# Kernel tuning notes

Measured on AMD Instinct MI355X. Metric: run time of the kernel, lower is better.

Reference implementation:

```python
import jax, jax.numpy as jnp
import numpy as np

WINDOW = 8
NUM_HEADS = 8
DIM = 256


def _relative_position_index(ws):
    coords = np.stack(np.meshgrid(np.arange(ws), np.arange(ws), indexing='ij'))  # [2,ws,ws]
    flat = coords.reshape(2, -1)  # [2, N]
    rel = flat[:, :, None] - flat[:, None, :]  # [2, N, N]
    rel = rel.transpose(1, 2, 0)  # [N, N, 2]
    rel[:, :, 0] += ws - 1
    rel[:, :, 1] += ws - 1
    rel[:, :, 0] *= 2 * ws - 1
    return rel.sum(-1).astype(np.int32)  # [N, N]


def setup_inputs() -> dict:
    key = jax.random.key(0)
    ks = jax.random.split(key, 6)
    B_, N, C = 4096, WINDOW * WINDOW, DIM
    return {
        'x': jax.random.normal(ks[0], (B_, N, C), jnp.float32),
        'qkv_w': jax.random.normal(ks[1], (3 * C, C), jnp.float32) * 0.02,
        'qkv_b': jax.random.normal(ks[2], (3 * C,), jnp.float32) * 0.02,
        'proj_w': jax.random.normal(ks[3], (C, C), jnp.float32) * 0.02,
        'proj_b': jax.random.normal(ks[4], (C,), jnp.float32) * 0.02,
        'bias_table': jax.random.normal(ks[5], ((2 * WINDOW - 1) ** 2, NUM_HEADS), jnp.float32) * 0.02,
        'rel_index': jnp.asarray(_relative_position_index(WINDOW)),
    }


def reference(x, qkv_w, qkv_b, proj_w, proj_b, bias_table, rel_index):
    B_, N, C = x.shape
    H = NUM_HEADS
    hd = C // H
    scale = hd ** -0.5
    qkv = x @ qkv_w.T + qkv_b  # [B_, N, 3C]
    qkv = qkv.reshape(B_, N, 3, H, hd).transpose(2, 0, 3, 1, 4)  # [3, B_, H, N, hd]
    q, k, v = qkv[0], qkv[1], qkv[2]
    attn = jnp.einsum('bhnd,bhmd->bhnm', q, k) * scale  # [B_, H, N, N]
    bias = bias_table[rel_index.reshape(-1)].reshape(N, N, H).transpose(2, 0, 1)  # [H, N, N]
    attn = jax.nn.softmax(attn + bias[None], axis=-1)
    out = jnp.einsum('bhnm,bhmd->bhnd', attn, v)  # [B_, H, N, hd]
    out = out.transpose(0, 2, 1, 3).reshape(B_, N, C)
    return out @ proj_w.T + proj_b
```

## Files before the change

kernel.cpp:

```cpp
#include <hip/hip_runtime.h>
#include <hip/hip_bf16.h>


typedef __attribute__((ext_vector_type(8))) short bf16x8;
typedef __attribute__((ext_vector_type(4))) float f32x4;

struct alignas(8) us4 { unsigned short x, y, z, w; };

__device__ inline unsigned short f2bf(float f) {
    unsigned u = __builtin_bit_cast(unsigned, f);
    u += 0x7fffu + ((u >> 16) & 1u);
    return (unsigned short)(u >> 16);
}

__device__ inline f32x4 mfma16(bf16x8 a, bf16x8 b, f32x4 c) {
    return __builtin_amdgcn_mfma_f32_16x16x32_bf16(a, b, c, 0, 0, 0);
}

__device__ inline bf16x8 lds8(const unsigned short* p) {
    return *reinterpret_cast<const bf16x8*>(p);
}

__global__ void prep_kernel(const float* __restrict__ qkv_w,
                            const float* __restrict__ proj_w,
                            const float* __restrict__ bias_table,
                            const int*   __restrict__ rel_index,
                            unsigned short* __restrict__ qkv_wb,
                            unsigned short* __restrict__ proj_wb,
                            float* __restrict__ biasF) {
    int stride = gridDim.x * blockDim.x;
    int t0 = blockIdx.x * blockDim.x + threadIdx.x;
    for (int i = t0; i < 768 * 256; i += stride) qkv_wb[i] = f2bf(qkv_w[i]);
    for (int i = t0; i < 256 * 256; i += stride) proj_wb[i] = f2bf(proj_w[i]);
    for (int i = t0; i < 8 * 64 * 64; i += stride) {
        int h = i >> 12, rem = i & 4095, m = rem >> 6, n = rem & 63;
        biasF[i] = bias_table[rel_index[m * 64 + n] * 8 + h];
    }
}

__global__ __launch_bounds__(512, 2) void win_attn_kernel(
    const float* __restrict__ x,
    const float* __restrict__ qkv_b,
    const float* __restrict__ proj_b,
    const unsigned short* __restrict__ qkv_wb,
    const unsigned short* __restrict__ proj_wb,
    const float* __restrict__ biasF,
    float* __restrict__ out)
{
    __shared__ unsigned short sm[76288];
    const int tid  = threadIdx.x;
    const int wid  = tid >> 6;
    const int lane = tid & 63;
    const int r16  = lane & 15;
    const int g    = lane >> 4;
    const int win  = blockIdx.x;
    const float* xg = x + (size_t)win * 16384;

#pragma unroll
    for (int i = 0; i < 8; ++i) {
        int flat = i * 2048 + tid * 4;
        float4 v = *reinterpret_cast<const float4*>(xg + flat);
        int row = flat >> 8, col = flat & 255;
        us4 pk = { f2bf(v.x), f2bf(v.y), f2bf(v.z), f2bf(v.w) };
        *reinterpret_cast<us4*>(&sm[row * 264 + col]) = pk;
    }
    __syncthreads();

    const int h = wid;
    int ntb[6];
    ntb[0] = 2 * h;      ntb[1] = 2 * h + 1;
    ntb[2] = 16 + 2 * h; ntb[3] = 17 + 2 * h;
    ntb[4] = 32 + 2 * h; ntb[5] = 33 + 2 * h;

    const f32x4 zero4 = {0.f, 0.f, 0.f, 0.f};
    f32x4 acc[4][6];
#pragma unroll
    for (int a = 0; a < 4; ++a)
#pragma unroll
        for (int b = 0; b < 6; ++b) acc[a][b] = zero4;

#pragma unroll
    for (int ks = 0; ks < 8; ++ks) {
        bf16x8 af[4];
#pragma unroll
        for (int mt = 0; mt < 4; ++mt)
            af[mt] = lds8(&sm[(mt * 16 + r16) * 264 + ks * 32 + g * 8]);
#pragma unroll
        for (int ni = 0; ni < 6; ++ni) {
            const unsigned short* wp =
                qkv_wb + (ntb[ni] * 16 + r16) * 256 + ks * 32 + g * 8;
            bf16x8 bf = *reinterpret_cast<const bf16x8*>(wp);
#pragma unroll
            for (int mt = 0; mt < 4; ++mt)
                acc[mt][ni] = mfma16(af[mt], bf, acc[mt][ni]);
        }
    }

    const int qbase = 16896 + h * 5120;
    const int kbase = qbase + 2560;
    const int vtb   = 57856 + h * 2304;

#pragma unroll
    for (int ni = 0; ni < 6; ++ni) {
        int n = ntb[ni] * 16 + r16;
        float qb = qkv_b[n];
        int d = (ni & 1) * 16 + r16;
#pragma unroll
        for (int mt = 0; mt < 4; ++mt) {
            f32x4 a4 = acc[mt][ni];
            if (ni < 2) {
#pragma unroll
                for (int j = 0; j < 4; ++j)
                    sm[qbase + (mt * 16 + g * 4 + j) * 40 + d] = f2bf(a4[j] + qb);
            } else if (ni < 4) {
#pragma unroll
                for (int j = 0; j < 4; ++j)
                    sm[kbase + (mt * 16 + g * 4 + j) * 40 + d] = f2bf(a4[j] + qb);
            } else {
                us4 pk = { f2bf(a4[0] + qb), f2bf(a4[1] + qb),
                           f2bf(a4[2] + qb), f2bf(a4[3] + qb) };
                *reinterpret_cast<us4*>(&sm[vtb + d * 72 + mt * 16 + g * 4]) = pk;
            }
        }
    }
    __syncthreads();

    bf16x8 ak[4], bq[4];
#pragma unroll
    for (int t = 0; t < 4; ++t) {
        ak[t] = lds8(&sm[kbase + (t * 16 + r16) * 40 + g * 8]);
        bq[t] = lds8(&sm[qbase + (t * 16 + r16) * 40 + g * 8]);
    }
    f32x4 st[4][4];
#pragma unroll
    for (int rt = 0; rt < 4; ++rt)
#pragma unroll
        for (int ct = 0; ct < 4; ++ct)
            st[rt][ct] = mfma16(ak[rt], bq[ct], zero4);

    const float scale = 0.1767766952966369f;
    const float* bh = biasF + h * 4096;

#pragma unroll
    for (int ct = 0; ct < 4; ++ct) {
        int m = ct * 16 + r16;
        float pv[4][4];
        float mx = -1e30f;
#pragma unroll
        for (int rt = 0; rt < 4; ++rt) {
            float4 b4 = *reinterpret_cast<const float4*>(bh + m * 64 + rt * 16 + g * 4);
            float bb[4] = { b4.x, b4.y, b4.z, b4.w };
#pragma unroll
            for (int j = 0; j < 4; ++j) {
                float v = st[rt][ct][j] * scale + bb[j];
                pv[rt][j] = v;
                mx = fmaxf(mx, v);
            }
        }
        mx = fmaxf(mx, __shfl_xor(mx, 16));
        mx = fmaxf(mx, __shfl_xor(mx, 32));
        float s = 0.f;
#pragma unroll
        for (int rt = 0; rt < 4; ++rt)
#pragma unroll
            for (int j = 0; j < 4; ++j) {
                float e = __expf(pv[rt][j] - mx);
                pv[rt][j] = e;
                s += e;
            }
        s += __shfl_xor(s, 16);
        s += __shfl_xor(s, 32);
        float inv = 1.f / s;
#pragma unroll
        for (int rt = 0; rt < 4; ++rt) {
            us4 pk = { f2bf(pv[rt][0] * inv), f2bf(pv[rt][1] * inv),
                       f2bf(pv[rt][2] * inv), f2bf(pv[rt][3] * inv) };
            *reinterpret_cast<us4*>(&sm[qbase + m * 72 + rt * 16 + g * 4]) = pk;
        }
    }
    asm volatile("s_waitcnt lgkmcnt(0)" ::: "memory");

    f32x4 o[4][2];
#pragma unroll
    for (int mt = 0; mt < 4; ++mt)
#pragma unroll
        for (int nt = 0; nt < 2; ++nt) o[mt][nt] = zero4;
#pragma unroll
    for (int ks = 0; ks < 2; ++ks) {
        bf16x8 ap[4];
#pragma unroll
        for (int mt = 0; mt < 4; ++mt)
            ap[mt] = lds8(&sm[qbase + (mt * 16 + r16) * 72 + ks * 32 + g * 8]);
#pragma unroll
        for (int nt = 0; nt < 2; ++nt) {
            bf16x8 bv = lds8(&sm[vtb + (nt * 16 + r16) * 72 + ks * 32 + g * 8]);
#pragma unroll
            for (int mt = 0; mt < 4; ++mt)
                o[mt][nt] = mfma16(ap[mt], bv, o[mt][nt]);
        }
    }
#pragma unroll
    for (int mt = 0; mt < 4; ++mt)
#pragma unroll
        for (int nt = 0; nt < 2; ++nt)
#pragma unroll
            for (int j = 0; j < 4; ++j)
                sm[(mt * 16 + g * 4 + j) * 264 + h * 32 + nt * 16 + r16] =
                    f2bf(o[mt][nt][j]);
    __syncthreads();

    f32x4 c3[4][2];
#pragma unroll
    for (int mt = 0; mt < 4; ++mt)
#pragma unroll
        for (int nt = 0; nt < 2; ++nt) c3[mt][nt] = zero4;
#pragma unroll
    for (int ks = 0; ks < 8; ++ks) {
        bf16x8 a3[4];
#pragma unroll
        for (int mt = 0; mt < 4; ++mt)
            a3[mt] = lds8(&sm[(mt * 16 + r16) * 264 + ks * 32 + g * 8]);
#pragma unroll
        for (int nt = 0; nt < 2; ++nt) {
            const unsigned short* wp =
                proj_wb + (wid * 32 + nt * 16 + r16) * 256 + ks * 32 + g * 8;
            bf16x8 b3 = *reinterpret_cast<const bf16x8*>(wp);
#pragma unroll
            for (int mt = 0; mt < 4; ++mt)
                c3[mt][nt] = mfma16(a3[mt], b3, c3[mt][nt]);
        }
    }
    float* og = out + (size_t)win * 16384;
#pragma unroll
    for (int nt = 0; nt < 2; ++nt) {
        int n = wid * 32 + nt * 16 + r16;
        float pb = proj_b[n];
#pragma unroll
        for (int mt = 0; mt < 4; ++mt)
#pragma unroll
            for (int j = 0; j < 4; ++j)
                og[(size_t)(mt * 16 + g * 4 + j) * 256 + n] = c3[mt][nt][j] + pb;
    }
}

extern "C" void kernel_launch(void* const* d_in, const int* in_sizes, int n_in,
                              void* d_out, int out_size, void* d_ws, size_t ws_size,
                              hipStream_t stream) {
    const float* x          = (const float*)d_in[0];
    const float* qkv_w      = (const float*)d_in[1];
    const float* qkv_b      = (const float*)d_in[2];
    const float* proj_w     = (const float*)d_in[3];
    const float* proj_b     = (const float*)d_in[4];
    const float* bias_table = (const float*)d_in[5];
    const int*   rel_index  = (const int*)d_in[6];

    unsigned short* qkv_wb = (unsigned short*)d_ws;
    unsigned short* proj_wb = (unsigned short*)((char*)d_ws + 393216);
    float* biasF = (float*)((char*)d_ws + 524288);

    prep_kernel<<<256, 256, 0, stream>>>(qkv_w, proj_w, bias_table, rel_index,
                                         qkv_wb, proj_wb, biasF);
    win_attn_kernel<<<4096, 512, 0, stream>>>(x, qkv_b, proj_b, qkv_wb, proj_wb,
                                              biasF, (float*)d_out);
}
```

Before: 426.3 us.

## Make attention kernel persistent over 16 windows with register prefetch and 16 waves

The kernel now runs 256 blocks of 1024 threads, and each block loops over 16 consecutive windows instead of handling one window per block. The next window's x tile is loaded into registers during the attention phase and written to LDS at the end of the iteration, so global loads overlap with compute. Work is split across 16 waves: two waves per head, each computing half of the Q/K/V columns and half of the query rows, and each wave computes a 16-column slice of the output projection. In exchange, each window needs more barriers, each wave holds fewer accumulators (less per-wave reuse), and carrying the prefetch registers raises register pressure.

After: 517.0 us. 21.3% more time.

```diff
diff --git a/kernel.cpp b/kernel.cpp
--- a/kernel.cpp
+++ b/kernel.cpp
@@ -38,7 +38,7 @@
     }
 }
 
-__global__ __launch_bounds__(512, 2) void win_attn_kernel(
+__global__ __launch_bounds__(1024, 4) void win_attn_kernel(
     const float* __restrict__ x,
     const float* __restrict__ qkv_b,
     const float* __restrict__ proj_b,
@@ -53,193 +53,211 @@
     const int lane = tid & 63;
     const int r16  = lane & 15;
     const int g    = lane >> 4;
-    const int win  = blockIdx.x;
-    const float* xg = x + (size_t)win * 16384;
-
-#pragma unroll
-    for (int i = 0; i < 8; ++i) {
-        int flat = i * 2048 + tid * 4;
-        float4 v = *reinterpret_cast<const float4*>(xg + flat);
-        int row = flat >> 8, col = flat & 255;
-        us4 pk = { f2bf(v.x), f2bf(v.y), f2bf(v.z), f2bf(v.w) };
-        *reinterpret_cast<us4*>(&sm[row * 264 + col]) = pk;
-    }
-    __syncthreads();
-
-    const int h = wid;
-    int ntb[6];
-    ntb[0] = 2 * h;      ntb[1] = 2 * h + 1;
-    ntb[2] = 16 + 2 * h; ntb[3] = 17 + 2 * h;
-    ntb[4] = 32 + 2 * h; ntb[5] = 33 + 2 * h;
-
+    const int h    = wid & 7;
+    const int hf   = wid >> 3;
     const f32x4 zero4 = {0.f, 0.f, 0.f, 0.f};
-    f32x4 acc[4][6];
-#pragma unroll
-    for (int a = 0; a < 4; ++a)
-#pragma unroll
-        for (int b = 0; b < 6; ++b) acc[a][b] = zero4;
-
-#pragma unroll
-    for (int ks = 0; ks < 8; ++ks) {
-        bf16x8 af[4];
-#pragma unroll
-        for (int mt = 0; mt < 4; ++mt)
-            af[mt] = lds8(&sm[(mt * 16 + r16) * 264 + ks * 32 + g * 8]);
-#pragma unroll
-        for (int ni = 0; ni < 6; ++ni) {
-            const unsigned short* wp =
-                qkv_wb + (ntb[ni] * 16 + r16) * 256 + ks * 32 + g * 8;
-            bf16x8 bf = *reinterpret_cast<const bf16x8*>(wp);
-#pragma unroll
-            for (int mt = 0; mt < 4; ++mt)
-                acc[mt][ni] = mfma16(af[mt], bf, acc[mt][ni]);
-        }
-    }
 
     const int qbase = 16896 + h * 5120;
     const int kbase = qbase + 2560;
     const int vtb   = 57856 + h * 2304;
 
-#pragma unroll
-    for (int ni = 0; ni < 6; ++ni) {
-        int n = ntb[ni] * 16 + r16;
-        float qb = qkv_b[n];
-        int d = (ni & 1) * 16 + r16;
-#pragma unroll
-        for (int mt = 0; mt < 4; ++mt) {
-            f32x4 a4 = acc[mt][ni];
-            if (ni < 2) {
+    const int ntb[3] = { 2 * h + hf, 16 + 2 * h + hf, 32 + 2 * h + hf };
+
+    const int win0 = blockIdx.x * 16;
+
+    float4 pf[4];
+#pragma unroll
+    for (int i = 0; i < 4; ++i)
+        pf[i] = *reinterpret_cast<const float4*>(
+            x + (size_t)win0 * 16384 + i * 4096 + tid * 4);
+#pragma unroll
+    for (int i = 0; i < 4; ++i) {
+        int flat = i * 4096 + tid * 4;
+        us4 pk = { f2bf(pf[i].x), f2bf(pf[i].y), f2bf(pf[i].z), f2bf(pf[i].w) };
+        *reinterpret_cast<us4*>(&sm[(flat >> 8) * 264 + (flat & 255)]) = pk;
+    }
+
+    for (int widx = 0; widx < 16; ++widx) {
+        const int win = win0 + widx;
+        __syncthreads();
+
+        f32x4 acc[4][3];
+#pragma unroll
+        for (int a = 0; a < 4; ++a)
+#pragma unroll
+            for (int b = 0; b < 3; ++b) acc[a][b] = zero4;
+
+#pragma unroll
+        for (int ks = 0; ks < 8; ++ks) {
+            bf16x8 af[4];
+#pragma unroll
+            for (int mt = 0; mt < 4; ++mt)
+                af[mt] = lds8(&sm[(mt * 16 + r16) * 264 + ks * 32 + g * 8]);
+#pragma unroll
+            for (int ni = 0; ni < 3; ++ni) {
+                bf16x8 bf = *reinterpret_cast<const bf16x8*>(
+                    qkv_wb + (ntb[ni] * 16 + r16) * 256 + ks * 32 + g * 8);
+#pragma unroll
+                for (int mt = 0; mt < 4; ++mt)
+                    acc[mt][ni] = mfma16(af[mt], bf, acc[mt][ni]);
+            }
+        }
+
+        const int d = hf * 16 + r16;
+#pragma unroll
+        for (int ni = 0; ni < 3; ++ni) {
+            float qb = qkv_b[ntb[ni] * 16 + r16];
+#pragma unroll
+            for (int mt = 0; mt < 4; ++mt) {
+                f32x4 a4 = acc[mt][ni];
+                if (ni == 0) {
+#pragma unroll
+                    for (int j = 0; j < 4; ++j)
+                        sm[qbase + (mt * 16 + g * 4 + j) * 40 + d] = f2bf(a4[j] + qb);
+                } else if (ni == 1) {
+#pragma unroll
+                    for (int j = 0; j < 4; ++j)
+                        sm[kbase + (mt * 16 + g * 4 + j) * 40 + d] = f2bf(a4[j] + qb);
+                } else {
+                    us4 pk = { f2bf(a4[0] + qb), f2bf(a4[1] + qb),
+                               f2bf(a4[2] + qb), f2bf(a4[3] + qb) };
+                    *reinterpret_cast<us4*>(&sm[vtb + d * 72 + mt * 16 + g * 4]) = pk;
+                }
+            }
+        }
+        __syncthreads();
+
+        if (widx < 15) {
+#pragma unroll
+            for (int i = 0; i < 4; ++i)
+                pf[i] = *reinterpret_cast<const float4*>(
+                    x + (size_t)(win + 1) * 16384 + i * 4096 + tid * 4);
+        }
+
+        bf16x8 ak[4], bq[2];
+#pragma unroll
+        for (int t = 0; t < 4; ++t)
+            ak[t] = lds8(&sm[kbase + (t * 16 + r16) * 40 + g * 8]);
+#pragma unroll
+        for (int c = 0; c < 2; ++c)
+            bq[c] = lds8(&sm[qbase + ((2 * hf + c) * 16 + r16) * 40 + g * 8]);
+
+        f32x4 st[4][2];
+#pragma unroll
+        for (int rt = 0; rt < 4; ++rt)
+#pragma unroll
+            for (int c = 0; c < 2; ++c)
+                st[rt][c] = mfma16(ak[rt], bq[c], zero4);
+        __syncthreads();
+
+        const float scale = 0.1767766952966369f;
+        const float* bh = biasF + h * 4096;
+
+#pragma unroll
+        for (int c = 0; c < 2; ++c) {
+            int m = (2 * hf + c) * 16 + r16;
+            float pv[4][4];
+            float mx = -1e30f;
+#pragma unroll
+            for (int rt = 0; rt < 4; ++rt) {
+                float4 b4 = *reinterpret_cast<const float4*>(
+                    bh + m * 64 + rt * 16 + g * 4);
+                float bb[4] = { b4.x, b4.y, b4.z, b4.w };
+#pragma unroll
+                for (int j = 0; j < 4; ++j) {
+                    float v = st[rt][c][j] * scale + bb[j];
+                    pv[rt][j] = v;
+                    mx = fmaxf(mx, v);
+                }
+            }
+            mx = fmaxf(mx, __shfl_xor(mx, 16));
+            mx = fmaxf(mx, __shfl_xor(mx, 32));
+            float s = 0.f;
+#pragma unroll
+            for (int rt = 0; rt < 4; ++rt)
+#pragma unroll
+                for (int j = 0; j < 4; ++j) {
+                    float e = __expf(pv[rt][j] - mx);
+                    pv[rt][j] = e;
+                    s += e;
+                }
+            s += __shfl_xor(s, 16);
+            s += __shfl_xor(s, 32);
+            float inv = 1.f / s;
+#pragma unroll
+            for (int rt = 0; rt < 4; ++rt) {
+                us4 pk = { f2bf(pv[rt][0] * inv), f2bf(pv[rt][1] * inv),
+                           f2bf(pv[rt][2] * inv), f2bf(pv[rt][3] * inv) };
+                *reinterpret_cast<us4*>(&sm[qbase + m * 72 + rt * 16 + g * 4]) = pk;
+            }
+        }
+        asm volatile("s_waitcnt lgkmcnt(0)" ::: "memory");
+
+        f32x4 o[2][2];
+#pragma unroll
+        for (int a = 0; a < 2; ++a)
+#pragma unroll
+            for (int b = 0; b < 2; ++b) o[a][b] = zero4;
+#pragma unroll
+        for (int ks = 0; ks < 2; ++ks) {
+            bf16x8 ap[2];
+#pragma unroll
+            for (int mtl = 0; mtl < 2; ++mtl)
+                ap[mtl] = lds8(&sm[qbase + ((2 * hf + mtl) * 16 + r16) * 72
+                                   + ks * 32 + g * 8]);
+#pragma unroll
+            for (int nt = 0; nt < 2; ++nt) {
+                bf16x8 bv = lds8(&sm[vtb + (nt * 16 + r16) * 72 + ks * 32 + g * 8]);
+#pragma unroll
+                for (int mtl = 0; mtl < 2; ++mtl)
+                    o[mtl][nt] = mfma16(ap[mtl], bv, o[mtl][nt]);
+            }
+        }
+#pragma unroll
+        for (int mtl = 0; mtl < 2; ++mtl)
+#pragma unroll
+            for (int nt = 0; nt < 2; ++nt)
 #pragma unroll
                 for (int j = 0; j < 4; ++j)
-                    sm[qbase + (mt * 16 + g * 4 + j) * 40 + d] = f2bf(a4[j] + qb);
-            } else if (ni < 4) {
+                    sm[((2 * hf + mtl) * 16 + g * 4 + j) * 264
+                       + h * 32 + nt * 16 + r16] = f2bf(o[mtl][nt][j]);
+        __syncthreads();
+
+        f32x4 c3[4];
+#pragma unroll
+        for (int mt = 0; mt < 4; ++mt) c3[mt] = zero4;
+#pragma unroll
+        for (int ks = 0; ks < 8; ++ks) {
+            bf16x8 b3 = *reinterpret_cast<const bf16x8*>(
+                proj_wb + (wid * 16 + r16) * 256 + ks * 32 + g * 8);
+#pragma unroll
+            for (int mt = 0; mt < 4; ++mt) {
+                bf16x8 a3 = lds8(&sm[(mt * 16 + r16) * 264 + ks * 32 + g * 8]);
+                c3[mt] = mfma16(a3, b3, c3[mt]);
+            }
+        }
+        __syncthreads();
+
+        float* og = out + (size_t)win * 16384;
+        {
+            int n = wid * 16 + r16;
+            float pb = proj_b[n];
+#pragma unroll
+            for (int mt = 0; mt < 4; ++mt)
 #pragma unroll
                 for (int j = 0; j < 4; ++j)
-                    sm[kbase + (mt * 16 + g * 4 + j) * 40 + d] = f2bf(a4[j] + qb);
-            } else {
-                us4 pk = { f2bf(a4[0] + qb), f2bf(a4[1] + qb),
-                           f2bf(a4[2] + qb), f2bf(a4[3] + qb) };
-                *reinterpret_cast<us4*>(&sm[vtb + d * 72 + mt * 16 + g * 4]) = pk;
-            }
-        }
-    }
-    __syncthreads();
-
-    bf16x8 ak[4], bq[4];
-#pragma unroll
-    for (int t = 0; t < 4; ++t) {
-        ak[t] = lds8(&sm[kbase + (t * 16 + r16) * 40 + g * 8]);
-        bq[t] = lds8(&sm[qbase + (t * 16 + r16) * 40 + g * 8]);
-    }
-    f32x4 st[4][4];
-#pragma unroll
-    for (int rt = 0; rt < 4; ++rt)
-#pragma unroll
-        for (int ct = 0; ct < 4; ++ct)
-            st[rt][ct] = mfma16(ak[rt], bq[ct], zero4);
-
-    const float scale = 0.1767766952966369f;
-    const float* bh = biasF + h * 4096;
-
-#pragma unroll
-    for (int ct = 0; ct < 4; ++ct) {
-        int m = ct * 16 + r16;
-        float pv[4][4];
-        float mx = -1e30f;
-#pragma unroll
-        for (int rt = 0; rt < 4; ++rt) {
-            float4 b4 = *reinterpret_cast<const float4*>(bh + m * 64 + rt * 16 + g * 4);
-            float bb[4] = { b4.x, b4.y, b4.z, b4.w };
-#pragma unroll
-            for (int j = 0; j < 4; ++j) {
-                float v = st[rt][ct][j] * scale + bb[j];
-                pv[rt][j] = v;
-                mx = fmaxf(mx, v);
-            }
-        }
-        mx = fmaxf(mx, __shfl_xor(mx, 16));
-        mx = fmaxf(mx, __shfl_xor(mx, 32));
-        float s = 0.f;
-#pragma unroll
-        for (int rt = 0; rt < 4; ++rt)
-#pragma unroll
-            for (int j = 0; j < 4; ++j) {
-                float e = __expf(pv[rt][j] - mx);
-                pv[rt][j] = e;
-                s += e;
-            }
-        s += __shfl_xor(s, 16);
-        s += __shfl_xor(s, 32);
-        float inv = 1.f / s;
-#pragma unroll
-        for (int rt = 0; rt < 4; ++rt) {
-            us4 pk = { f2bf(pv[rt][0] * inv), f2bf(pv[rt][1] * inv),
-                       f2bf(pv[rt][2] * inv), f2bf(pv[rt][3] * inv) };
-            *reinterpret_cast<us4*>(&sm[qbase + m * 72 + rt * 16 + g * 4]) = pk;
-        }
-    }
-    asm volatile("s_waitcnt lgkmcnt(0)" ::: "memory");
-
-    f32x4 o[4][2];
-#pragma unroll
-    for (int mt = 0; mt < 4; ++mt)
-#pragma unroll
-        for (int nt = 0; nt < 2; ++nt) o[mt][nt] = zero4;
-#pragma unroll
-    for (int ks = 0; ks < 2; ++ks) {
-        bf16x8 ap[4];
-#pragma unroll
-        for (int mt = 0; mt < 4; ++mt)
-            ap[mt] = lds8(&sm[qbase + (mt * 16 + r16) * 72 + ks * 32 + g * 8]);
-#pragma unroll
-        for (int nt = 0; nt < 2; ++nt) {
-            bf16x8 bv = lds8(&sm[vtb + (nt * 16 + r16) * 72 + ks * 32 + g * 8]);
-#pragma unroll
-            for (int mt = 0; mt < 4; ++mt)
-                o[mt][nt] = mfma16(ap[mt], bv, o[mt][nt]);
-        }
-    }
-#pragma unroll
-    for (int mt = 0; mt < 4; ++mt)
-#pragma unroll
-        for (int nt = 0; nt < 2; ++nt)
-#pragma unroll
-            for (int j = 0; j < 4; ++j)
-                sm[(mt * 16 + g * 4 + j) * 264 + h * 32 + nt * 16 + r16] =
-                    f2bf(o[mt][nt][j]);
-    __syncthreads();
-
-    f32x4 c3[4][2];
-#pragma unroll
-    for (int mt = 0; mt < 4; ++mt)
-#pragma unroll
-        for (int nt = 0; nt < 2; ++nt) c3[mt][nt] = zero4;
-#pragma unroll
-    for (int ks = 0; ks < 8; ++ks) {
-        bf16x8 a3[4];
-#pragma unroll
-        for (int mt = 0; mt < 4; ++mt)
-            a3[mt] = lds8(&sm[(mt * 16 + r16) * 264 + ks * 32 + g * 8]);
-#pragma unroll
-        for (int nt = 0; nt < 2; ++nt) {
-            const unsigned short* wp =
-                proj_wb + (wid * 32 + nt * 16 + r16) * 256 + ks * 32 + g * 8;
-            bf16x8 b3 = *reinterpret_cast<const bf16x8*>(wp);
-#pragma unroll
-            for (int mt = 0; mt < 4; ++mt)
-                c3[mt][nt] = mfma16(a3[mt], b3, c3[mt][nt]);
-        }
-    }
-    float* og = out + (size_t)win * 16384;
-#pragma unroll
-    for (int nt = 0; nt < 2; ++nt) {
-        int n = wid * 32 + nt * 16 + r16;
-        float pb = proj_b[n];
-#pragma unroll
-        for (int mt = 0; mt < 4; ++mt)
-#pragma unroll
-            for (int j = 0; j < 4; ++j)
-                og[(size_t)(mt * 16 + g * 4 + j) * 256 + n] = c3[mt][nt][j] + pb;
+                    og[(size_t)(mt * 16 + g * 4 + j) * 256 + n] = c3[mt][j] + pb;
+        }
+
+        if (widx < 15) {
+#pragma unroll
+            for (int i = 0; i < 4; ++i) {
+                int flat = i * 4096 + tid * 4;
+                us4 pk = { f2bf(pf[i].x), f2bf(pf[i].y),
+                           f2bf(pf[i].z), f2bf(pf[i].w) };
+                *reinterpret_cast<us4*>(&sm[(flat >> 8) * 264 + (flat & 255)]) = pk;
+            }
+        }
     }
 }
 
@@ -254,12 +272,12 @@
     const float* bias_table = (const float*)d_in[5];
     const int*   rel_index  = (const int*)d_in[6];
 
-    unsigned short* qkv_wb = (unsigned short*)d_ws;
+    unsigned short* qkv_wb  = (unsigned short*)d_ws;
     unsigned short* proj_wb = (unsigned short*)((char*)d_ws + 393216);
-    float* biasF = (float*)((char*)d_ws + 524288);
+    float* biasF            = (float*)((char*)d_ws + 524288);
 
     prep_kernel<<<256, 256, 0, stream>>>(qkv_w, proj_w, bias_table, rel_index,
                                          qkv_wb, proj_wb, biasF);
-    win_attn_kernel<<<4096, 512, 0, stream>>>(x, qkv_b, proj_b, qkv_wb, proj_wb,
+    win_attn_kernel<<<256, 1024, 0, stream>>>(x, qkv_b, proj_b, qkv_wb, proj_wb,
                                               biasF, (float*)d_out);
 }
```

## Keep Q/K/V and softmax probabilities in registers via lane shuffles instead of LDS

Applied to the files above, without the earlier changes.

Computes Q, K and V per head in three separate register-resident GEMM passes, choosing operand order so that the MFMA accumulator layouts can be repacked into MFMA input fragments with xor-shuffle butterflies rather than round-tripping through shared memory. The attention scale is folded into the K weights and bias during prep, and the relative position bias is used as the MFMA accumulator initialiser. Shared memory drops to the x tile plus the attention output tile, and launch bounds are raised so more blocks can fit per CU. The tradeoffs are extra cross-lane shuffles, higher register pressure under the tighter launch bound, and possible spills.

Result: slower. 621.9 us (+45.9%).

```diff
diff --git a/kernel.cpp b/kernel.cpp
--- a/kernel.cpp
+++ b/kernel.cpp
@@ -13,12 +13,36 @@
     return (unsigned short)(u >> 16);
 }
 
+__device__ inline unsigned pack2(float lo, float hi) {
+    return (unsigned)f2bf(lo) | ((unsigned)f2bf(hi) << 16);
+}
+
 __device__ inline f32x4 mfma16(bf16x8 a, bf16x8 b, f32x4 c) {
     return __builtin_amdgcn_mfma_f32_16x16x32_bf16(a, b, c, 0, 0, 0);
 }
 
 __device__ inline bf16x8 lds8(const unsigned short* p) {
     return *reinterpret_cast<const bf16x8*>(p);
+}
+
+__device__ inline void bfly_stage(unsigned V[4], int D, bool b) {
+    unsigned t0 = (unsigned)__shfl_xor((int)V[0], D);
+    unsigned t1 = (unsigned)__shfl_xor((int)V[1], D);
+    unsigned t2 = (unsigned)__shfl_xor((int)V[2], D);
+    unsigned t3 = (unsigned)__shfl_xor((int)V[3], D);
+    V[0] = b ? t2 : V[0];
+    V[1] = b ? t3 : V[1];
+    V[2] = b ? V[2] : t0;
+    V[3] = b ? V[3] : t1;
+}
+
+__device__ inline bf16x8 bfly4(unsigned v0, unsigned v1, unsigned v2,
+                               unsigned v3, int lane) {
+    unsigned V[4] = { v0, v1, v2, v3 };
+    bfly_stage(V, 32, (lane & 32) != 0);
+    bfly_stage(V, 16, (lane & 16) != 0);
+    uint4 r = { V[0], V[1], V[2], V[3] };
+    return __builtin_bit_cast(bf16x8, r);
 }
 
 __global__ void prep_kernel(const float* __restrict__ qkv_w,
@@ -28,9 +52,15 @@
                             unsigned short* __restrict__ qkv_wb,
                             unsigned short* __restrict__ proj_wb,
                             float* __restrict__ biasF) {
+    const float scale = 0.1767766952966369f;
     int stride = gridDim.x * blockDim.x;
     int t0 = blockIdx.x * blockDim.x + threadIdx.x;
-    for (int i = t0; i < 768 * 256; i += stride) qkv_wb[i] = f2bf(qkv_w[i]);
+    for (int i = t0; i < 768 * 256; i += stride) {
+        float w = qkv_w[i];
+        int row = i >> 8;
+        if (row >= 256 && row < 512) w *= scale;
+        qkv_wb[i] = f2bf(w);
+    }
     for (int i = t0; i < 256 * 256; i += stride) proj_wb[i] = f2bf(proj_w[i]);
     for (int i = t0; i < 8 * 64 * 64; i += stride) {
         int h = i >> 12, rem = i & 4095, m = rem >> 6, n = rem & 63;
@@ -38,7 +68,7 @@
     }
 }
 
-__global__ __launch_bounds__(512, 2) void win_attn_kernel(
+__global__ __launch_bounds__(512, 4) void win_attn_kernel(
     const float* __restrict__ x,
     const float* __restrict__ qkv_b,
     const float* __restrict__ proj_b,
@@ -47,116 +77,165 @@
     const float* __restrict__ biasF,
     float* __restrict__ out)
 {
-    __shared__ unsigned short sm[76288];
+    __shared__ unsigned short sm[33792];
+    const int AO   = 16896;
     const int tid  = threadIdx.x;
     const int wid  = tid >> 6;
     const int lane = tid & 63;
     const int r16  = lane & 15;
     const int g    = lane >> 4;
+    const int h    = wid;
     const int win  = blockIdx.x;
+
+    const float* bh = biasF + h * 4096;
+    const f32x4 zero4 = {0.f, 0.f, 0.f, 0.f};
+
     const float* xg = x + (size_t)win * 16384;
-
 #pragma unroll
     for (int i = 0; i < 8; ++i) {
         int flat = i * 2048 + tid * 4;
         float4 v = *reinterpret_cast<const float4*>(xg + flat);
-        int row = flat >> 8, col = flat & 255;
         us4 pk = { f2bf(v.x), f2bf(v.y), f2bf(v.z), f2bf(v.w) };
-        *reinterpret_cast<us4*>(&sm[row * 264 + col]) = pk;
+        *reinterpret_cast<us4*>(&sm[(flat >> 8) * 264 + (flat & 255)]) = pk;
     }
     __syncthreads();
 
-    const int h = wid;
-    int ntb[6];
-    ntb[0] = 2 * h;      ntb[1] = 2 * h + 1;
-    ntb[2] = 16 + 2 * h; ntb[3] = 17 + 2 * h;
-    ntb[4] = 32 + 2 * h; ntb[5] = 33 + 2 * h;
-
-    const f32x4 zero4 = {0.f, 0.f, 0.f, 0.f};
-    f32x4 acc[4][6];
-#pragma unroll
-    for (int a = 0; a < 4; ++a)
-#pragma unroll
-        for (int b = 0; b < 6; ++b) acc[a][b] = zero4;
-
-#pragma unroll
-    for (int ks = 0; ks < 8; ++ks) {
-        bf16x8 af[4];
-#pragma unroll
-        for (int mt = 0; mt < 4; ++mt)
-            af[mt] = lds8(&sm[(mt * 16 + r16) * 264 + ks * 32 + g * 8]);
-#pragma unroll
-        for (int ni = 0; ni < 6; ++ni) {
-            const unsigned short* wp =
-                qkv_wb + (ntb[ni] * 16 + r16) * 256 + ks * 32 + g * 8;
-            bf16x8 bf = *reinterpret_cast<const bf16x8*>(wp);
-#pragma unroll
-            for (int mt = 0; mt < 4; ++mt)
-                acc[mt][ni] = mfma16(af[mt], bf, acc[mt][ni]);
-        }
-    }
-
-    const int qbase = 16896 + h * 5120;
-    const int kbase = qbase + 2560;
-    const int vtb   = 57856 + h * 2304;
-
-#pragma unroll
-    for (int ni = 0; ni < 6; ++ni) {
-        int n = ntb[ni] * 16 + r16;
-        float qb = qkv_b[n];
-        int d = (ni & 1) * 16 + r16;
-#pragma unroll
-        for (int mt = 0; mt < 4; ++mt) {
-            f32x4 a4 = acc[mt][ni];
-            if (ni < 2) {
+    unsigned qp[4][2][2];
+    {
+        f32x4 acc[4][2];
+#pragma unroll
+        for (int t = 0; t < 4; ++t)
+#pragma unroll
+            for (int dt = 0; dt < 2; ++dt) {
+                f32x4 ci;
 #pragma unroll
                 for (int j = 0; j < 4; ++j)
-                    sm[qbase + (mt * 16 + g * 4 + j) * 40 + d] = f2bf(a4[j] + qb);
-            } else if (ni < 4) {
+                    ci[j] = qkv_b[(2 * h + dt) * 16 + g * 4 + j];
+                acc[t][dt] = ci;
+            }
+#pragma unroll
+        for (int ks = 0; ks < 8; ++ks) {
+            bf16x8 xf[4];
+#pragma unroll
+            for (int t = 0; t < 4; ++t)
+                xf[t] = lds8(&sm[(t * 16 + r16) * 264 + ks * 32 + g * 8]);
+            bf16x8 w0 = *reinterpret_cast<const bf16x8*>(
+                qkv_wb + ((2 * h + 0) * 16 + r16) * 256 + ks * 32 + g * 8);
+            bf16x8 w1 = *reinterpret_cast<const bf16x8*>(
+                qkv_wb + ((2 * h + 1) * 16 + r16) * 256 + ks * 32 + g * 8);
+#pragma unroll
+            for (int t = 0; t < 4; ++t) {
+                acc[t][0] = mfma16(w0, xf[t], acc[t][0]);
+                acc[t][1] = mfma16(w1, xf[t], acc[t][1]);
+            }
+        }
+#pragma unroll
+        for (int t = 0; t < 4; ++t)
+#pragma unroll
+            for (int dt = 0; dt < 2; ++dt) {
+                qp[t][dt][0] = pack2(acc[t][dt][0], acc[t][dt][1]);
+                qp[t][dt][1] = pack2(acc[t][dt][2], acc[t][dt][3]);
+            }
+    }
+
+    unsigned kp[4][2][2];
+    {
+        f32x4 acc[4][2];
+#pragma unroll
+        for (int t = 0; t < 4; ++t)
+#pragma unroll
+            for (int dt = 0; dt < 2; ++dt) {
+                f32x4 ci;
 #pragma unroll
                 for (int j = 0; j < 4; ++j)
-                    sm[kbase + (mt * 16 + g * 4 + j) * 40 + d] = f2bf(a4[j] + qb);
-            } else {
-                us4 pk = { f2bf(a4[0] + qb), f2bf(a4[1] + qb),
-                           f2bf(a4[2] + qb), f2bf(a4[3] + qb) };
-                *reinterpret_cast<us4*>(&sm[vtb + d * 72 + mt * 16 + g * 4]) = pk;
-            }
-        }
-    }
-    __syncthreads();
-
-    bf16x8 ak[4], bq[4];
-#pragma unroll
-    for (int t = 0; t < 4; ++t) {
-        ak[t] = lds8(&sm[kbase + (t * 16 + r16) * 40 + g * 8]);
-        bq[t] = lds8(&sm[qbase + (t * 16 + r16) * 40 + g * 8]);
-    }
-    f32x4 st[4][4];
-#pragma unroll
-    for (int rt = 0; rt < 4; ++rt)
-#pragma unroll
-        for (int ct = 0; ct < 4; ++ct)
-            st[rt][ct] = mfma16(ak[rt], bq[ct], zero4);
-
-    const float scale = 0.1767766952966369f;
-    const float* bh = biasF + h * 4096;
-
-#pragma unroll
-    for (int ct = 0; ct < 4; ++ct) {
-        int m = ct * 16 + r16;
-        float pv[4][4];
+                    ci[j] = qkv_b[256 + (2 * h + dt) * 16 + g * 4 + j]
+                            * 0.1767766952966369f;
+                acc[t][dt] = ci;
+            }
+#pragma unroll
+        for (int ks = 0; ks < 8; ++ks) {
+            bf16x8 xf[4];
+#pragma unroll
+            for (int t = 0; t < 4; ++t)
+                xf[t] = lds8(&sm[(t * 16 + r16) * 264 + ks * 32 + g * 8]);
+            bf16x8 w0 = *reinterpret_cast<const bf16x8*>(
+                qkv_wb + ((16 + 2 * h + 0) * 16 + r16) * 256 + ks * 32 + g * 8);
+            bf16x8 w1 = *reinterpret_cast<const bf16x8*>(
+                qkv_wb + ((16 + 2 * h + 1) * 16 + r16) * 256 + ks * 32 + g * 8);
+#pragma unroll
+            for (int t = 0; t < 4; ++t) {
+                acc[t][0] = mfma16(w0, xf[t], acc[t][0]);
+                acc[t][1] = mfma16(w1, xf[t], acc[t][1]);
+            }
+        }
+#pragma unroll
+        for (int t = 0; t < 4; ++t)
+#pragma unroll
+            for (int dt = 0; dt < 2; ++dt) {
+                kp[t][dt][0] = pack2(acc[t][dt][0], acc[t][dt][1]);
+                kp[t][dt][1] = pack2(acc[t][dt][2], acc[t][dt][3]);
+            }
+    }
+
+    unsigned vp[4][2][2];
+    {
+        f32x4 acc[4][2];
+#pragma unroll
+        for (int t = 0; t < 4; ++t)
+#pragma unroll
+            for (int dt = 0; dt < 2; ++dt) {
+                float vb = qkv_b[512 + (2 * h + dt) * 16 + r16];
+                f32x4 ci = { vb, vb, vb, vb };
+                acc[t][dt] = ci;
+            }
+#pragma unroll
+        for (int ks = 0; ks < 8; ++ks) {
+            bf16x8 xf[4];
+#pragma unroll
+            for (int t = 0; t < 4; ++t)
+                xf[t] = lds8(&sm[(t * 16 + r16) * 264 + ks * 32 + g * 8]);
+            bf16x8 w0 = *reinterpret_cast<const bf16x8*>(
+                qkv_wb + ((32 + 2 * h + 0) * 16 + r16) * 256 + ks * 32 + g * 8);
+            bf16x8 w1 = *reinterpret_cast<const bf16x8*>(
+                qkv_wb + ((32 + 2 * h + 1) * 16 + r16) * 256 + ks * 32 + g * 8);
+#pragma unroll
+            for (int t = 0; t < 4; ++t) {
+                acc[t][0] = mfma16(xf[t], w0, acc[t][0]);
+                acc[t][1] = mfma16(xf[t], w1, acc[t][1]);
+            }
+        }
+#pragma unroll
+        for (int t = 0; t < 4; ++t)
+#pragma unroll
+            for (int dt = 0; dt < 2; ++dt) {
+                vp[t][dt][0] = pack2(acc[t][dt][0], acc[t][dt][1]);
+                vp[t][dt][1] = pack2(acc[t][dt][2], acc[t][dt][3]);
+            }
+    }
+
+    bf16x8 ak[4];
+#pragma unroll
+    for (int t = 0; t < 4; ++t)
+        ak[t] = bfly4(kp[t][0][0], kp[t][0][1], kp[t][1][0], kp[t][1][1], lane);
+
+    bf16x8 ap[4][2];
+#pragma unroll
+    for (int c = 0; c < 4; ++c) {
+        bf16x8 bqc = bfly4(qp[c][0][0], qp[c][0][1], qp[c][1][0], qp[c][1][1],
+                           lane);
+        f32x4 stc[4];
+#pragma unroll
+        for (int rt = 0; rt < 4; ++rt) {
+            float4 b4 = *reinterpret_cast<const float4*>(
+                bh + (c * 16 + r16) * 64 + rt * 16 + g * 4);
+            f32x4 ci = { b4.x, b4.y, b4.z, b4.w };
+            stc[rt] = mfma16(ak[rt], bqc, ci);
+        }
         float mx = -1e30f;
 #pragma unroll
-        for (int rt = 0; rt < 4; ++rt) {
-            float4 b4 = *reinterpret_cast<const float4*>(bh + m * 64 + rt * 16 + g * 4);
-            float bb[4] = { b4.x, b4.y, b4.z, b4.w };
-#pragma unroll
-            for (int j = 0; j < 4; ++j) {
-                float v = st[rt][ct][j] * scale + bb[j];
-                pv[rt][j] = v;
-                mx = fmaxf(mx, v);
-            }
-        }
+        for (int rt = 0; rt < 4; ++rt)
+#pragma unroll
+            for (int j = 0; j < 4; ++j) mx = fmaxf(mx, stc[rt][j]);
         mx = fmaxf(mx, __shfl_xor(mx, 16));
         mx = fmaxf(mx, __shfl_xor(mx, 32));
         float s = 0.f;
@@ -164,49 +243,54 @@
         for (int rt = 0; rt < 4; ++rt)
 #pragma unroll
             for (int j = 0; j < 4; ++j) {
-                float e = __expf(pv[rt][j] - mx);
-                pv[rt][j] = e;
+                float e = __expf(stc[rt][j] - mx);
+                stc[rt][j] = e;
                 s += e;
             }
         s += __shfl_xor(s, 16);
         s += __shfl_xor(s, 32);
         float inv = 1.f / s;
+        unsigned pp[4][2];
 #pragma unroll
         for (int rt = 0; rt < 4; ++rt) {
-            us4 pk = { f2bf(pv[rt][0] * inv), f2bf(pv[rt][1] * inv),
-                       f2bf(pv[rt][2] * inv), f2bf(pv[rt][3] * inv) };
-            *reinterpret_cast<us4*>(&sm[qbase + m * 72 + rt * 16 + g * 4]) = pk;
-        }
-    }
-    asm volatile("s_waitcnt lgkmcnt(0)" ::: "memory");
-
-    f32x4 o[4][2];
-#pragma unroll
-    for (int mt = 0; mt < 4; ++mt)
-#pragma unroll
-        for (int nt = 0; nt < 2; ++nt) o[mt][nt] = zero4;
-#pragma unroll
-    for (int ks = 0; ks < 2; ++ks) {
-        bf16x8 ap[4];
-#pragma unroll
-        for (int mt = 0; mt < 4; ++mt)
-            ap[mt] = lds8(&sm[qbase + (mt * 16 + r16) * 72 + ks * 32 + g * 8]);
-#pragma unroll
-        for (int nt = 0; nt < 2; ++nt) {
-            bf16x8 bv = lds8(&sm[vtb + (nt * 16 + r16) * 72 + ks * 32 + g * 8]);
-#pragma unroll
-            for (int mt = 0; mt < 4; ++mt)
-                o[mt][nt] = mfma16(ap[mt], bv, o[mt][nt]);
-        }
-    }
-#pragma unroll
-    for (int mt = 0; mt < 4; ++mt)
-#pragma unroll
-        for (int nt = 0; nt < 2; ++nt)
-#pragma unroll
-            for (int j = 0; j < 4; ++j)
-                sm[(mt * 16 + g * 4 + j) * 264 + h * 32 + nt * 16 + r16] =
-                    f2bf(o[mt][nt][j]);
+            pp[rt][0] = pack2(stc[rt][0] * inv, stc[rt][1] * inv);
+            pp[rt][1] = pack2(stc[rt][2] * inv, stc[rt][3] * inv);
+        }
+        ap[c][0] = bfly4(pp[0][0], pp[0][1], pp[1][0], pp[1][1], lane);
+        ap[c][1] = bfly4(pp[2][0], pp[2][1], pp[3][0], pp[3][1], lane);
+    }
+
+    bf16x8 av[2][2];
+#pragma unroll
+    for (int dt = 0; dt < 2; ++dt)
+#pragma unroll
+        for (int ks = 0; ks < 2; ++ks)
+            av[dt][ks] = bfly4(vp[2 * ks][dt][0], vp[2 * ks][dt][1],
+                               vp[2 * ks + 1][dt][0], vp[2 * ks + 1][dt][1],
+                               lane);
+
+    f32x4 o2[2][4];
+#pragma unroll
+    for (int dt = 0; dt < 2; ++dt)
+#pragma unroll
+        for (int mq = 0; mq < 4; ++mq) o2[dt][mq] = zero4;
+#pragma unroll
+    for (int ks = 0; ks < 2; ++ks)
+#pragma unroll
+        for (int dt = 0; dt < 2; ++dt)
+#pragma unroll
+            for (int mq = 0; mq < 4; ++mq)
+                o2[dt][mq] = mfma16(av[dt][ks], ap[mq][ks], o2[dt][mq]);
+
+#pragma unroll
+    for (int dt = 0; dt < 2; ++dt)
+#pragma unroll
+        for (int mq = 0; mq < 4; ++mq) {
+            us4 pk = { f2bf(o2[dt][mq][0]), f2bf(o2[dt][mq][1]),
+                       f2bf(o2[dt][mq][2]), f2bf(o2[dt][mq][3]) };
+            *reinterpret_cast<us4*>(
+                &sm[AO + (mq * 16 + r16) * 264 + h * 32 + dt * 16 + g * 4]) = pk;
+        }
     __syncthreads();
 
     f32x4 c3[4][2];
@@ -219,12 +303,11 @@
         bf16x8 a3[4];
 #pragma unroll
         for (int mt = 0; mt < 4; ++mt)
-            a3[mt] = lds8(&sm[(mt * 16 + r16) * 264 + ks * 32 + g * 8]);
+            a3[mt] = lds8(&sm[AO + (mt * 16 + r16) * 264 + ks * 32 + g * 8]);
 #pragma unroll
         for (int nt = 0; nt < 2; ++nt) {
-            const unsigned short* wp =
-                proj_wb + (wid * 32 + nt * 16 + r16) * 256 + ks * 32 + g * 8;
-            bf16x8 b3 = *reinterpret_cast<const bf16x8*>(wp);
+            bf16x8 b3 = *reinterpret_cast<const bf16x8*>(
+                proj_wb + (wid * 32 + nt * 16 + r16) * 256 + ks * 32 + g * 8);
 #pragma unroll
             for (int mt = 0; mt < 4; ++mt)
                 c3[mt][nt] = mfma16(a3[mt], b3, c3[mt][nt]);
@@ -254,9 +337,9 @@
     const float* bias_table = (const float*)d_in[5];
     const int*   rel_index  = (const int*)d_in[6];
 
-    unsigned short* qkv_wb = (unsigned short*)d_ws;
+    unsigned short* qkv_wb  = (unsigned short*)d_ws;
     unsigned short* proj_wb = (unsigned short*)((char*)d_ws + 393216);
-    float* biasF = (float*)((char*)d_ws + 524288);
+    float* biasF            = (float*)((char*)d_ws + 524288);
 
     prep_kernel<<<256, 256, 0, stream>>>(qkv_w, proj_w, bias_table, rel_index,
                                          qkv_wb, proj_wb, biasF);
```
